# Kernel tuning notes

Measured on AMD Instinct MI355X. Metric: run time of the kernel, lower is better.

The kernel has to match this reference:

```python
import jax, jax.numpy as jnp
import numpy as np

NUM_HEADS = 8
HEAD_DIM = 64
SR = 2
LN_EPS = 1e-5


def _ln(x, g, b):
    # LayerNorm over last dim (torch nn.LayerNorm, eps=1e-5)
    m = jnp.mean(x, axis=-1, keepdims=True)
    v = jnp.var(x, axis=-1, keepdims=True)
    return (x - m) * jax.lax.rsqrt(v + LN_EPS) * g + b


def setup_inputs() -> dict:
    key = jax.random.key(0)
    ks = jax.random.split(key, 8)
    B, N, C = 8, 4096, 512
    Cc = 512                      # cross_dim
    inner = NUM_HEADS * HEAD_DIM  # 512
    w = lambda k, shp: jax.random.normal(k, shp, jnp.float32) * 0.02
    return {
        "x": jax.random.normal(ks[0], (B, N, C), jnp.float32),
        "y": jax.random.normal(ks[1], (B, 64 * 64, Cc), jnp.float32),
        "Wq": w(ks[2], (C, inner)),
        "Wkv": w(ks[3], (Cc, 2 * inner)),
        "Wproj": w(ks[4], (inner, C)),
        "bproj": jnp.zeros((C,), jnp.float32),
        "g_cross": jnp.ones((Cc,), jnp.float32),
        "b_cross": jnp.zeros((Cc,), jnp.float32),
        "sr_w": w(ks[5], (SR, SR, Cc, Cc)),   # HWIO conv kernel
        "sr_b": jnp.zeros((Cc,), jnp.float32),
        "g_sr": jnp.ones((Cc,), jnp.float32),
        "b_sr": jnp.zeros((Cc,), jnp.float32),
        "y_H": 64,
        "y_W": 64,
    }


def reference(x, y, Wq, Wkv, Wproj, bproj, g_cross, b_cross, sr_w, sr_b, g_sr, b_sr, y_H, y_W):
    B, N, C = x.shape
    h, d = NUM_HEADS, HEAD_DIM
    inner = h * d
    scale = d ** -0.5

    # q projection: [B, h, N, d]
    q = (x @ Wq).reshape(B, N, h, d).transpose(0, 2, 1, 3)

    # cross-attention norm on context
    y = _ln(y, g_cross, b_cross)
    Cc = y.shape[-1]

    # spatial reduction: conv(kernel=stride=SR) over [B, y_H, y_W, Cc]
    x_ = y.reshape(B, y_H, y_W, Cc)
    x_ = jax.lax.conv_general_dilated(
        x_, sr_w, window_strides=(SR, SR), padding='VALID',
        dimension_numbers=('NHWC', 'HWIO', 'NHWC')) + sr_b
    Nk = (y_H // SR) * (y_W // SR)
    x_ = _ln(x_.reshape(B, Nk, Cc), g_sr, b_sr)

    # kv projection: [2, B, h, Nk, d]
    kv = (x_ @ Wkv).reshape(B, Nk, 2, h, d).transpose(2, 0, 3, 1, 4)
    k, v = kv[0], kv[1]

    attn = jax.nn.softmax(jnp.einsum('bhnd,bhmd->bhnm', q, k) * scale, axis=-1)
    out = jnp.einsum('bhnm,bhmd->bhnd', attn, v)          # [B, h, N, d]
    out = out.transpose(0, 2, 1, 3).reshape(B, N, inner)  # [B, N, inner]
    return out @ Wproj + bproj
```

## Files before the change

kernel.cpp:

```cpp
#include <hip/hip_runtime.h>
#include <stdint.h>

typedef unsigned short u16;
typedef __attribute__((ext_vector_type(8))) short bf16x8;
typedef __attribute__((ext_vector_type(8))) unsigned short u16x8;
typedef __attribute__((ext_vector_type(4))) float f32x4;
typedef __attribute__((ext_vector_type(16))) float f32x16;
typedef __attribute__((ext_vector_type(4))) unsigned short u16x4;
typedef __attribute__((ext_vector_type(2))) unsigned int uint2v;

__device__ __forceinline__ u16 f2bf(float f) {
  unsigned u = __float_as_uint(f);
  u += 0x7fffu + ((u >> 16) & 1u);
  return (u16)(u >> 16);
}

__device__ __forceinline__ unsigned cvtpk(float lo, float hi) {
  unsigned r;
  asm("v_cvt_pk_bf16_f32 %0, %1, %2" : "=v"(r) : "v"(lo), "v"(hi));
  return r;
}

__device__ __forceinline__ void gload16(const u16* g, u16* l) {
  __builtin_amdgcn_global_load_lds(
      (const __attribute__((address_space(1))) unsigned int*)(uintptr_t)g,
      (__attribute__((address_space(3))) unsigned int*)(uintptr_t)l, 16, 0, 0);
}

__global__ __launch_bounds__(256) void transpose4_bf16(
    const float* __restrict__ W0, const float* __restrict__ W1,
    const float* __restrict__ W2, const float* __restrict__ W3,
    u16* __restrict__ T0, u16* __restrict__ T1, u16* __restrict__ T2,
    u16* __restrict__ T3) {
  __shared__ u16 lds[64][66];
  const float* W;
  u16* T;
  int R, C;
  switch (blockIdx.y) {
    case 0: W = W0; T = T0; R = 512; C = 512; break;
    case 1: W = W1; T = T1; R = 512; C = 1024; break;
    case 2: W = W2; T = T2; R = 512; C = 512; break;
    default: W = W3; T = T3; R = 2048; C = 512; break;
  }
  const int tilesC = C >> 6;
  const int nt = (R >> 6) * tilesC;
  const int tile = blockIdx.x;
  if (tile >= nt) return;
  const int tr = tile / tilesC, tc = tile - tr * tilesC;
  const int r0 = tr << 6, c0 = tc << 6;
  const int t = threadIdx.x;
  const int rr = t >> 2, cq = (t & 3) << 4;
  const float* src = W + (size_t)(r0 + rr) * C + c0 + cq;
  unsigned* ldsrow = (unsigned*)&lds[rr][cq];
#pragma unroll
  for (int j = 0; j < 4; j++) {
    f32x4 v = *(const f32x4*)(src + j * 4);
    ldsrow[j * 2] = cvtpk(v.x, v.y);
    ldsrow[j * 2 + 1] = cvtpk(v.z, v.w);
  }
  __syncthreads();
  const int oc = t >> 2, rq = (t & 3) << 4;
  u16x8 o0, o1;
#pragma unroll
  for (int j = 0; j < 8; j++) {
    o0[j] = lds[rq + j][oc];
    o1[j] = lds[rq + 8 + j][oc];
  }
  u16* dst = T + (size_t)(c0 + oc) * R + r0 + rq;
  *(u16x8*)dst = o0;
  *(u16x8*)(dst + 8) = o1;
}

__global__ __launch_bounds__(256) void cvt_bf16(const float* __restrict__ in,
                                                u16* __restrict__ out, int n4) {
  int i = blockIdx.x * 256 + threadIdx.x;
  if (i >= n4) return;
  f32x4 v = *(const f32x4*)(in + (size_t)i * 4);
  u16x4 o;
  o.x = f2bf(v.x); o.y = f2bf(v.y); o.z = f2bf(v.z); o.w = f2bf(v.w);
  *(u16x4*)(out + (size_t)i * 4) = o;
}

__global__ __launch_bounds__(256) void ln_y_im2col(
    const float* __restrict__ y, const float* __restrict__ g,
    const float* __restrict__ bb, u16* __restrict__ patches) {
  int row = blockIdx.x * 4 + (threadIdx.x >> 6);
  int l = threadIdx.x & 63;
  const float* yr = y + (size_t)row * 512;
  f32x4 v0 = *(const f32x4*)(yr + l * 4);
  f32x4 v1 = *(const f32x4*)(yr + 256 + l * 4);
  float s = v0.x + v0.y + v0.z + v0.w + v1.x + v1.y + v1.z + v1.w;
  float ss = v0.x * v0.x + v0.y * v0.y + v0.z * v0.z + v0.w * v0.w +
             v1.x * v1.x + v1.y * v1.y + v1.z * v1.z + v1.w * v1.w;
#pragma unroll
  for (int m = 1; m <= 32; m <<= 1) {
    s += __shfl_xor(s, m);
    ss += __shfl_xor(ss, m);
  }
  float mean = s * (1.0f / 512.0f);
  float inv = rsqrtf(ss * (1.0f / 512.0f) - mean * mean + 1e-5f);
  f32x4 g0 = *(const f32x4*)(g + l * 4), g1 = *(const f32x4*)(g + 256 + l * 4);
  f32x4 c0 = *(const f32x4*)(bb + l * 4), c1 = *(const f32x4*)(bb + 256 + l * 4);
  f32x4 o0 = (v0 - mean) * inv * g0 + c0;
  f32x4 o1 = (v1 - mean) * inv * g1 + c1;
  int b = row >> 12, n = row & 4095, r = n >> 6, cc = n & 63;
  u16* dst = patches +
             (size_t)((b << 10) + ((r >> 1) << 5) + (cc >> 1)) * 2048 +
             ((r & 1) * 2 + (cc & 1)) * 512;
  u16x4 w0, w1;
  w0.x = f2bf(o0.x); w0.y = f2bf(o0.y); w0.z = f2bf(o0.z); w0.w = f2bf(o0.w);
  w1.x = f2bf(o1.x); w1.y = f2bf(o1.y); w1.z = f2bf(o1.z); w1.w = f2bf(o1.w);
  *(u16x4*)(dst + l * 4) = w0;
  *(u16x4*)(dst + 256 + l * 4) = w1;
}

__global__ __launch_bounds__(256) void ln_rows(
    const float* __restrict__ in, const float* __restrict__ g,
    const float* __restrict__ bb, u16* __restrict__ out) {
  int row = blockIdx.x * 4 + (threadIdx.x >> 6);
  int l = threadIdx.x & 63;
  const float* xr = in + (size_t)row * 512;
  f32x4 v0 = *(const f32x4*)(xr + l * 4);
  f32x4 v1 = *(const f32x4*)(xr + 256 + l * 4);
  float s = v0.x + v0.y + v0.z + v0.w + v1.x + v1.y + v1.z + v1.w;
  float ss = v0.x * v0.x + v0.y * v0.y + v0.z * v0.z + v0.w * v0.w +
             v1.x * v1.x + v1.y * v1.y + v1.z * v1.z + v1.w * v1.w;
#pragma unroll
  for (int m = 1; m <= 32; m <<= 1) {
    s += __shfl_xor(s, m);
    ss += __shfl_xor(ss, m);
  }
  float mean = s * (1.0f / 512.0f);
  float inv = rsqrtf(ss * (1.0f / 512.0f) - mean * mean + 1e-5f);
  f32x4 g0 = *(const f32x4*)(g + l * 4), g1 = *(const f32x4*)(g + 256 + l * 4);
  f32x4 c0 = *(const f32x4*)(bb + l * 4), c1 = *(const f32x4*)(bb + 256 + l * 4);
  f32x4 o0 = (v0 - mean) * inv * g0 + c0;
  f32x4 o1 = (v1 - mean) * inv * g1 + c1;
  u16* dst = out + (size_t)row * 512;
  u16x4 w0, w1;
  w0.x = f2bf(o0.x); w0.y = f2bf(o0.y); w0.z = f2bf(o0.z); w0.w = f2bf(o0.w);
  w1.x = f2bf(o1.x); w1.y = f2bf(o1.y); w1.z = f2bf(o1.z); w1.w = f2bf(o1.w);
  *(u16x4*)(dst + l * 4) = w0;
  *(u16x4*)(dst + 256 + l * 4) = w1;
}

template <int EPI>
__global__ __launch_bounds__(256) void gemm_bt(
    const u16* __restrict__ A, const u16* __restrict__ BT, int M, int N, int K,
    float* __restrict__ OF, u16* __restrict__ OB, const float* __restrict__ bias,
    float scale, u16* __restrict__ KB, u16* __restrict__ VT) {
  __shared__ u16 As[2][128 * 32];
  __shared__ u16 Bs[2][128 * 32];
  const int tid = threadIdx.x;
  const int l = tid & 63, w = tid >> 6;
  const int brow = blockIdx.y * 128, bcol = blockIdx.x * 128;
  const int wr = w >> 1, wc = w & 1;
  const int lr = l & 15, lk = (l >> 4) * 8;
  const int srow = l >> 2, scol = (l & 3) * 8;
  const int r0s = w * 32 + srow, r1s = w * 32 + 16 + srow;
  const u16* Ap0 = &A[(size_t)(brow + r0s) * K + scol];
  const u16* Ap1 = &A[(size_t)(brow + r1s) * K + scol];
  const u16* Bp0 = &BT[(size_t)(bcol + r0s) * K + scol];
  const u16* Bp1 = &BT[(size_t)(bcol + r1s) * K + scol];
  const int lo0 = r0s * 32 + scol, lo1 = r1s * 32 + scol;
  f32x4 acc[4][4] = {};
  const int nt = K >> 5;
  gload16(Ap0, &As[0][lo0]);
  gload16(Ap1, &As[0][lo1]);
  gload16(Bp0, &Bs[0][lo0]);
  gload16(Bp1, &Bs[0][lo1]);
  __syncthreads();
  int cur = 0;
  for (int t = 0; t < nt; ++t) {
    if (t + 1 < nt) {
      int k0 = (t + 1) << 5;
      gload16(Ap0 + k0, &As[cur ^ 1][lo0]);
      gload16(Ap1 + k0, &As[cur ^ 1][lo1]);
      gload16(Bp0 + k0, &Bs[cur ^ 1][lo0]);
      gload16(Bp1 + k0, &Bs[cur ^ 1][lo1]);
    }
    bf16x8 af[4], bfr[4];
#pragma unroll
    for (int m = 0; m < 4; m++)
      af[m] = *(const bf16x8*)&As[cur][(wr * 64 + m * 16 + lr) * 32 + lk];
#pragma unroll
    for (int n = 0; n < 4; n++)
      bfr[n] = *(const bf16x8*)&Bs[cur][(wc * 64 + n * 16 + lr) * 32 + lk];
#pragma unroll
    for (int m = 0; m < 4; m++)
#pragma unroll
      for (int n = 0; n < 4; n++)
        acc[m][n] = __builtin_amdgcn_mfma_f32_16x16x32_bf16(af[m], bfr[n],
                                                            acc[m][n], 0, 0, 0);
    __syncthreads();
    cur ^= 1;
  }
#pragma unroll
  for (int m = 0; m < 4; m++) {
    int r0 = brow + wr * 64 + m * 16 + (l >> 4) * 4;
#pragma unroll
    for (int n = 0; n < 4; n++) {
      int c = bcol + wc * 64 + n * 16 + lr;
#pragma unroll
      for (int j = 0; j < 4; j++) {
        float v = acc[m][n][j];
        int rrow = r0 + j;
        if (EPI == 0) {
          OF[(size_t)rrow * N + c] = v + bias[c];
        } else if (EPI == 2) {
          OB[(size_t)rrow * N + c] = f2bf(v * scale);
        } else {
          int b = rrow >> 10, nn = rrow & 1023;
          int dd = c & 63;
          if (c < 512) {
            int hh = c >> 6;
            KB[((size_t)((b * 8 + hh) * 1024 + nn)) * 64 + dd] = f2bf(v);
          } else {
            int hh = (c - 512) >> 6;
            VT[((size_t)((b * 8 + hh) * 64 + dd)) * 1024 + nn] = f2bf(v);
          }
        }
      }
    }
  }
}

__global__ __launch_bounds__(256) void gemm_bt64(
    const u16* __restrict__ A, const u16* __restrict__ BT, int M, int N, int K,
    float* __restrict__ OF, const float* __restrict__ bias) {
  __shared__ u16 As[2][64 * 32];
  __shared__ u16 Bs[2][128 * 32];
  const int tid = threadIdx.x;
  const int l = tid & 63, w = tid >> 6;
  const int brow = blockIdx.y * 64, bcol = blockIdx.x * 128;
  const int lr = l & 15, lk = (l >> 4) * 8;
  const int srow = tid >> 2, scol = (tid & 3) * 8;
  const u16* Ap = &A[(size_t)(brow + srow) * K + scol];
  const u16* Bp0 = &BT[(size_t)(bcol + srow) * K + scol];
  const u16* Bp1 = &BT[(size_t)(bcol + 64 + srow) * K + scol];
  const int loA = srow * 32 + scol;
  const int loB1 = (64 + srow) * 32 + scol;
  f32x4 acc[4][2] = {};
  const int nt = K >> 5;
  gload16(Ap, &As[0][loA]);
  gload16(Bp0, &Bs[0][loA]);
  gload16(Bp1, &Bs[0][loB1]);
  __syncthreads();
  int cur = 0;
  for (int t = 0; t < nt; ++t) {
    if (t + 1 < nt) {
      int k0 = (t + 1) << 5;
      gload16(Ap + k0, &As[cur ^ 1][loA]);
      gload16(Bp0 + k0, &Bs[cur ^ 1][loA]);
      gload16(Bp1 + k0, &Bs[cur ^ 1][loB1]);
    }
    bf16x8 af[4], bfr[2];
#pragma unroll
    for (int m = 0; m < 4; m++)
      af[m] = *(const bf16x8*)&As[cur][(m * 16 + lr) * 32 + lk];
#pragma unroll
    for (int n = 0; n < 2; n++)
      bfr[n] = *(const bf16x8*)&Bs[cur][(w * 32 + n * 16 + lr) * 32 + lk];
#pragma unroll
    for (int m = 0; m < 4; m++)
#pragma unroll
      for (int n = 0; n < 2; n++)
        acc[m][n] = __builtin_amdgcn_mfma_f32_16x16x32_bf16(af[m], bfr[n],
                                                            acc[m][n], 0, 0, 0);
    __syncthreads();
    cur ^= 1;
  }
#pragma unroll
  for (int m = 0; m < 4; m++) {
    int r0 = brow + m * 16 + (l >> 4) * 4;
#pragma unroll
    for (int n = 0; n < 2; n++) {
      int c = bcol + w * 32 + n * 16 + lr;
#pragma unroll
      for (int j = 0; j < 4; j++)
        OF[(size_t)(r0 + j) * N + c] = acc[m][n][j] + bias[c];
    }
  }
}

__global__ __launch_bounds__(256) void attn_fwd(
    const u16* __restrict__ q, const u16* __restrict__ kb,
    const u16* __restrict__ vt, u16* __restrict__ o) {
  __shared__ u16 Ks[2][32 * 64];
  __shared__ u16 Vs[2][64 * 32];
  const int idx = blockIdx.x;
  const int bh = ((idx >> 7) << 3) | (idx & 7);
  const int qb = (idx >> 3) & 15;
  const int b = bh >> 3, h = bh & 7;
  const int tid = threadIdx.x;
  const int w = tid >> 6, l = tid & 63;
  const int lq = l & 31, hi = l >> 5;
  const int qrowA = qb * 256 + w * 64 + lq;
  const int qrowB = qrowA + 32;
  const u16* qpA = q + (size_t)((b << 12) + qrowA) * 512 + h * 64 + hi * 8;
  const u16* qpB = q + (size_t)((b << 12) + qrowB) * 512 + h * 64 + hi * 8;
  bf16x8 qfA[4], qfB[4];
#pragma unroll
  for (int ds = 0; ds < 4; ds++) {
    qfA[ds] = *(const bf16x8*)(qpA + ds * 16);
    qfB[ds] = *(const bf16x8*)(qpB + ds * 16);
  }
  const short one = 0x3F80;
  const bf16x8 ones = {one, one, one, one, one, one, one, one};
  const u16* kp = kb + (size_t)bh * 65536;
  const u16* vtb = vt + (size_t)bh * 65536;
  const int krow = tid >> 3, kslot = tid & 7;
  const u16* ksrc = kp + krow * 64 + ((kslot ^ (krow & 7)) << 3);
  const int vrow = tid >> 2, vslot = tid & 3;
  const u16* vsrc = vtb + (size_t)vrow * 1024 + ((vslot ^ ((vrow >> 1) & 3)) << 3);
  const int kOff0 = lq * 64;
  const int vOff0 = lq * 32;
  const int vOff1 = (lq + 32) * 32;
  const int vmask = (lq >> 1) & 3;
  f32x16 oA0 = {}, oA1 = {}, oB0 = {}, oB1 = {};
  f32x16 smA = {}, smB = {};
  gload16(ksrc, &Ks[0][tid << 3]);
  gload16(vsrc, &Vs[0][tid << 3]);
  __syncthreads();
  int cur = 0;
  for (int kv0 = 0; kv0 < 1024; kv0 += 32) {
    if (kv0 + 32 < 1024) {
      gload16(ksrc + (kv0 + 32) * 64, &Ks[cur ^ 1][tid << 3]);
      gload16(vsrc + (kv0 + 32), &Vs[cur ^ 1][tid << 3]);
    }
    bf16x8 kf[4];
#pragma unroll
    for (int ds = 0; ds < 4; ds++)
      kf[ds] = *(const bf16x8*)&Ks[cur][kOff0 + ((((ds << 1) + hi) ^ (lq & 7)) << 3)];
    bf16x8 vf0[2], vf1[2];
#pragma unroll
    for (int t = 0; t < 2; t++) {
      int sw = (((t << 1) + hi) ^ vmask) << 3;
      vf0[t] = *(const bf16x8*)&Vs[cur][vOff0 + sw];
      vf1[t] = *(const bf16x8*)&Vs[cur][vOff1 + sw];
    }
    f32x16 stA = {}, stB = {};
#pragma unroll
    for (int ds = 0; ds < 4; ds++) {
      stA = __builtin_amdgcn_mfma_f32_32x32x16_bf16(kf[ds], qfA[ds], stA, 0, 0, 0);
      stB = __builtin_amdgcn_mfma_f32_32x32x16_bf16(kf[ds], qfB[ds], stB, 0, 0, 0);
    }
    bf16x8 pbA[2], pbB[2];
#pragma unroll
    for (int tile = 0; tile < 2; tile++) {
      f32x16& st = tile ? stB : stA;
      bf16x8* pb = tile ? pbB : pbA;
      float p[16];
#pragma unroll
      for (int r = 0; r < 16; r++) p[r] = __builtin_amdgcn_exp2f(st[r]);
#pragma unroll
      for (int t = 0; t < 2; t++) {
        unsigned c0 = cvtpk(p[8 * t + 0], p[8 * t + 1]);
        unsigned c1 = cvtpk(p[8 * t + 2], p[8 * t + 3]);
        unsigned c2 = cvtpk(p[8 * t + 4], p[8 * t + 5]);
        unsigned c3 = cvtpk(p[8 * t + 6], p[8 * t + 7]);
        uint2v r02 = __builtin_amdgcn_permlane32_swap(c0, c2, false, false);
        uint2v r13 = __builtin_amdgcn_permlane32_swap(c1, c3, false, false);
        union {
          unsigned u[4];
          bf16x8 v;
        } pk;
        pk.u[0] = r02.x;
        pk.u[1] = r13.x;
        pk.u[2] = r02.y;
        pk.u[3] = r13.y;
        pb[t] = pk.v;
      }
    }
#pragma unroll
    for (int t = 0; t < 2; t++) {
      oA0 = __builtin_amdgcn_mfma_f32_32x32x16_bf16(vf0[t], pbA[t], oA0, 0, 0, 0);
      oA1 = __builtin_amdgcn_mfma_f32_32x32x16_bf16(vf1[t], pbA[t], oA1, 0, 0, 0);
      smA = __builtin_amdgcn_mfma_f32_32x32x16_bf16(ones, pbA[t], smA, 0, 0, 0);
      oB0 = __builtin_amdgcn_mfma_f32_32x32x16_bf16(vf0[t], pbB[t], oB0, 0, 0, 0);
      oB1 = __builtin_amdgcn_mfma_f32_32x32x16_bf16(vf1[t], pbB[t], oB1, 0, 0, 0);
      smB = __builtin_amdgcn_mfma_f32_32x32x16_bf16(ones, pbB[t], smB, 0, 0, 0);
    }
    __syncthreads();
    cur ^= 1;
  }
  const float invA = 1.0f / smA[0], invB = 1.0f / smB[0];
  u16* opA = o + (size_t)((b << 12) + qrowA) * 512 + h * 64;
  u16* opB = o + (size_t)((b << 12) + qrowB) * 512 + h * 64;
#pragma unroll
  for (int g = 0; g < 4; g++) {
    u16x4 a0, a1, b0, b1;
#pragma unroll
    for (int j = 0; j < 4; j++) {
      a0[j] = f2bf(oA0[g * 4 + j] * invA);
      a1[j] = f2bf(oA1[g * 4 + j] * invA);
      b0[j] = f2bf(oB0[g * 4 + j] * invB);
      b1[j] = f2bf(oB1[g * 4 + j] * invB);
    }
    *(u16x4*)(opA + 8 * g + 4 * hi) = a0;
    *(u16x4*)(opA + 32 + 8 * g + 4 * hi) = a1;
    *(u16x4*)(opB + 8 * g + 4 * hi) = b0;
    *(u16x4*)(opB + 32 + 8 * g + 4 * hi) = b1;
  }
}

extern "C" void kernel_launch(void* const* d_in, const int* in_sizes, int n_in,
                              void* d_out, int out_size, void* d_ws, size_t ws_size,
                              hipStream_t stream) {
  (void)in_sizes; (void)n_in; (void)out_size; (void)ws_size;
  const float* x = (const float*)d_in[0];
  const float* y = (const float*)d_in[1];
  const float* Wq = (const float*)d_in[2];
  const float* Wkv = (const float*)d_in[3];
  const float* Wproj = (const float*)d_in[4];
  const float* bproj = (const float*)d_in[5];
  const float* g_cross = (const float*)d_in[6];
  const float* b_cross = (const float*)d_in[7];
  const float* srw = (const float*)d_in[8];
  const float* sr_b = (const float*)d_in[9];
  const float* g_sr = (const float*)d_in[10];
  const float* b_sr = (const float*)d_in[11];
  float* out = (float*)d_out;

  u16* p = (u16*)d_ws;
  u16* WqT = p;    p += (size_t)512 * 512;
  u16* WkvT = p;   p += (size_t)1024 * 512;
  u16* WprojT = p; p += (size_t)512 * 512;
  u16* srwT = p;   p += (size_t)512 * 2048;
  u16* kbuf = p;   p += (size_t)8 * 8 * 1024 * 64;
  u16* vtbuf = p;  p += (size_t)8 * 8 * 1024 * 64;
  u16* xln = p;    p += (size_t)8192 * 512;
  u16* R1 = p;     p += (size_t)32768 * 512;
  u16* R2 = p;     p += (size_t)32768 * 512;
  u16* patches = R1;
  u16* xbf = R1;
  u16* attnb = R1;
  float* convout = (float*)R2;
  u16* qbuf = R2;

  transpose4_bf16<<<dim3(256, 4), 256, 0, stream>>>(Wq, Wkv, Wproj, srw,
                                                    WqT, WkvT, WprojT, srwT);
  ln_y_im2col<<<8192, 256, 0, stream>>>(y, g_cross, b_cross, patches);
  gemm_bt64<<<dim3(4, 128), 256, 0, stream>>>(patches, srwT, 8192, 512, 2048,
                                              convout, sr_b);
  ln_rows<<<2048, 256, 0, stream>>>(convout, g_sr, b_sr, xln);
  gemm_bt<1><<<dim3(8, 64), 256, 0, stream>>>(xln, WkvT, 8192, 1024, 512,
                                              nullptr, nullptr, nullptr, 1.0f,
                                              kbuf, vtbuf);
  cvt_bf16<<<16384, 256, 0, stream>>>(x, xbf, 32768 * 512 / 4);
  gemm_bt<2><<<dim3(4, 256), 256, 0, stream>>>(xbf, WqT, 32768, 512, 512,
                                               nullptr, qbuf, nullptr,
                                               0.125f * 1.44269504f,
                                               nullptr, nullptr);
  attn_fwd<<<dim3(1024), 256, 0, stream>>>(qbuf, kbuf, vtbuf, attnb);
  gemm_bt<0><<<dim3(4, 256), 256, 0, stream>>>(attnb, WprojT, 32768, 512, 512,
                                               out, nullptr, bproj, 1.0f,
                                               nullptr, nullptr);
}
```

Measured before the change: 277.6 us.

## Use triple-buffered LDS with vmcnt waits and one barrier per iteration

```diff
diff --git a/kernel.cpp b/kernel.cpp
--- a/kernel.cpp
+++ b/kernel.cpp
@@ -26,6 +26,11 @@
       (const __attribute__((address_space(1))) unsigned int*)(uintptr_t)g,
       (__attribute__((address_space(3))) unsigned int*)(uintptr_t)l, 16, 0, 0);
 }
+
+#define WAITV(N) asm volatile("s_waitcnt vmcnt(" #N ")" ::: "memory")
+#define BARRIER_FENCE()                  \
+  __builtin_amdgcn_s_barrier();          \
+  __builtin_amdgcn_sched_barrier(0)
 
 __global__ __launch_bounds__(256) void transpose4_bf16(
     const float* __restrict__ W0, const float* __restrict__ W1,
@@ -149,8 +154,8 @@
     const u16* __restrict__ A, const u16* __restrict__ BT, int M, int N, int K,
     float* __restrict__ OF, u16* __restrict__ OB, const float* __restrict__ bias,
     float scale, u16* __restrict__ KB, u16* __restrict__ VT) {
-  __shared__ u16 As[2][128 * 32];
-  __shared__ u16 Bs[2][128 * 32];
+  __shared__ u16 As[3][128 * 32];
+  __shared__ u16 Bs[3][128 * 32];
   const int tid = threadIdx.x;
   const int l = tid & 63, w = tid >> 6;
   const int brow = blockIdx.y * 128, bcol = blockIdx.x * 128;
@@ -169,31 +174,37 @@
   gload16(Ap1, &As[0][lo1]);
   gload16(Bp0, &Bs[0][lo0]);
   gload16(Bp1, &Bs[0][lo1]);
-  __syncthreads();
-  int cur = 0;
+  gload16(Ap0 + 32, &As[1][lo0]);
+  gload16(Ap1 + 32, &As[1][lo1]);
+  gload16(Bp0 + 32, &Bs[1][lo0]);
+  gload16(Bp1 + 32, &Bs[1][lo1]);
+  int bufC = 0, bufS = 2;
   for (int t = 0; t < nt; ++t) {
-    if (t + 1 < nt) {
-      int k0 = (t + 1) << 5;
-      gload16(Ap0 + k0, &As[cur ^ 1][lo0]);
-      gload16(Ap1 + k0, &As[cur ^ 1][lo1]);
-      gload16(Bp0 + k0, &Bs[cur ^ 1][lo0]);
-      gload16(Bp1 + k0, &Bs[cur ^ 1][lo1]);
+    if (t + 1 < nt) WAITV(4);
+    else WAITV(0);
+    BARRIER_FENCE();
+    if (t + 2 < nt) {
+      int k0 = (t + 2) << 5;
+      gload16(Ap0 + k0, &As[bufS][lo0]);
+      gload16(Ap1 + k0, &As[bufS][lo1]);
+      gload16(Bp0 + k0, &Bs[bufS][lo0]);
+      gload16(Bp1 + k0, &Bs[bufS][lo1]);
     }
     bf16x8 af[4], bfr[4];
 #pragma unroll
     for (int m = 0; m < 4; m++)
-      af[m] = *(const bf16x8*)&As[cur][(wr * 64 + m * 16 + lr) * 32 + lk];
+      af[m] = *(const bf16x8*)&As[bufC][(wr * 64 + m * 16 + lr) * 32 + lk];
 #pragma unroll
     for (int n = 0; n < 4; n++)
-      bfr[n] = *(const bf16x8*)&Bs[cur][(wc * 64 + n * 16 + lr) * 32 + lk];
+      bfr[n] = *(const bf16x8*)&Bs[bufC][(wc * 64 + n * 16 + lr) * 32 + lk];
 #pragma unroll
     for (int m = 0; m < 4; m++)
 #pragma unroll
       for (int n = 0; n < 4; n++)
         acc[m][n] = __builtin_amdgcn_mfma_f32_16x16x32_bf16(af[m], bfr[n],
                                                             acc[m][n], 0, 0, 0);
-    __syncthreads();
-    cur ^= 1;
+    bufC = bufC == 2 ? 0 : bufC + 1;
+    bufS = bufS == 2 ? 0 : bufS + 1;
   }
 #pragma unroll
   for (int m = 0; m < 4; m++) {
@@ -228,8 +239,8 @@
 __global__ __launch_bounds__(256) void gemm_bt64(
     const u16* __restrict__ A, const u16* __restrict__ BT, int M, int N, int K,
     float* __restrict__ OF, const float* __restrict__ bias) {
-  __shared__ u16 As[2][64 * 32];
-  __shared__ u16 Bs[2][128 * 32];
+  __shared__ u16 As[3][64 * 32];
+  __shared__ u16 Bs[3][128 * 32];
   const int tid = threadIdx.x;
   const int l = tid & 63, w = tid >> 6;
   const int brow = blockIdx.y * 64, bcol = blockIdx.x * 128;
@@ -245,30 +256,35 @@
   gload16(Ap, &As[0][loA]);
   gload16(Bp0, &Bs[0][loA]);
   gload16(Bp1, &Bs[0][loB1]);
-  __syncthreads();
-  int cur = 0;
+  gload16(Ap + 32, &As[1][loA]);
+  gload16(Bp0 + 32, &Bs[1][loA]);
+  gload16(Bp1 + 32, &Bs[1][loB1]);
+  int bufC = 0, bufS = 2;
   for (int t = 0; t < nt; ++t) {
-    if (t + 1 < nt) {
-      int k0 = (t + 1) << 5;
-      gload16(Ap + k0, &As[cur ^ 1][loA]);
-      gload16(Bp0 + k0, &Bs[cur ^ 1][loA]);
-      gload16(Bp1 + k0, &Bs[cur ^ 1][loB1]);
+    if (t + 1 < nt) WAITV(3);
+    else WAITV(0);
+    BARRIER_FENCE();
+    if (t + 2 < nt) {
+      int k0 = (t + 2) << 5;
+      gload16(Ap + k0, &As[bufS][loA]);
+      gload16(Bp0 + k0, &Bs[bufS][loA]);
+      gload16(Bp1 + k0, &Bs[bufS][loB1]);
     }
     bf16x8 af[4], bfr[2];
 #pragma unroll
     for (int m = 0; m < 4; m++)
-      af[m] = *(const bf16x8*)&As[cur][(m * 16 + lr) * 32 + lk];
+      af[m] = *(const bf16x8*)&As[bufC][(m * 16 + lr) * 32 + lk];
 #pragma unroll
     for (int n = 0; n < 2; n++)
-      bfr[n] = *(const bf16x8*)&Bs[cur][(w * 32 + n * 16 + lr) * 32 + lk];
+      bfr[n] = *(const bf16x8*)&Bs[bufC][(w * 32 + n * 16 + lr) * 32 + lk];
 #pragma unroll
     for (int m = 0; m < 4; m++)
 #pragma unroll
       for (int n = 0; n < 2; n++)
         acc[m][n] = __builtin_amdgcn_mfma_f32_16x16x32_bf16(af[m], bfr[n],
                                                             acc[m][n], 0, 0, 0);
-    __syncthreads();
-    cur ^= 1;
+    bufC = bufC == 2 ? 0 : bufC + 1;
+    bufS = bufS == 2 ? 0 : bufS + 1;
   }
 #pragma unroll
   for (int m = 0; m < 4; m++) {
@@ -286,8 +302,8 @@
 __global__ __launch_bounds__(256) void attn_fwd(
     const u16* __restrict__ q, const u16* __restrict__ kb,
     const u16* __restrict__ vt, u16* __restrict__ o) {
-  __shared__ u16 Ks[2][32 * 64];
-  __shared__ u16 Vs[2][64 * 32];
+  __shared__ u16 Ks[3][32 * 64];
+  __shared__ u16 Vs[3][64 * 32];
   const int idx = blockIdx.x;
   const int bh = ((idx >> 7) << 3) | (idx & 7);
   const int qb = (idx >> 3) & 15;
@@ -321,23 +337,30 @@
   f32x16 smA = {}, smB = {};
   gload16(ksrc, &Ks[0][tid << 3]);
   gload16(vsrc, &Vs[0][tid << 3]);
-  __syncthreads();
-  int cur = 0;
-  for (int kv0 = 0; kv0 < 1024; kv0 += 32) {
-    if (kv0 + 32 < 1024) {
-      gload16(ksrc + (kv0 + 32) * 64, &Ks[cur ^ 1][tid << 3]);
-      gload16(vsrc + (kv0 + 32), &Vs[cur ^ 1][tid << 3]);
-    }
+  gload16(ksrc + 32 * 64, &Ks[1][tid << 3]);
+  gload16(vsrc + 32, &Vs[1][tid << 3]);
+  int bufC = 0, bufS = 2;
+  for (int it = 0; it < 32; ++it) {
+    if (it < 31) WAITV(2);
+    else WAITV(0);
+    BARRIER_FENCE();
+    if (it + 2 < 32) {
+      int kv2 = (it + 2) << 5;
+      gload16(ksrc + kv2 * 64, &Ks[bufS][tid << 3]);
+      gload16(vsrc + kv2, &Vs[bufS][tid << 3]);
+    }
+    const u16* Kc = Ks[bufC];
+    const u16* Vc = Vs[bufC];
     bf16x8 kf[4];
 #pragma unroll
     for (int ds = 0; ds < 4; ds++)
-      kf[ds] = *(const bf16x8*)&Ks[cur][kOff0 + ((((ds << 1) + hi) ^ (lq & 7)) << 3)];
+      kf[ds] = *(const bf16x8*)&Kc[kOff0 + ((((ds << 1) + hi) ^ (lq & 7)) << 3)];
     bf16x8 vf0[2], vf1[2];
 #pragma unroll
     for (int t = 0; t < 2; t++) {
       int sw = (((t << 1) + hi) ^ vmask) << 3;
-      vf0[t] = *(const bf16x8*)&Vs[cur][vOff0 + sw];
-      vf1[t] = *(const bf16x8*)&Vs[cur][vOff1 + sw];
+      vf0[t] = *(const bf16x8*)&Vc[vOff0 + sw];
+      vf1[t] = *(const bf16x8*)&Vc[vOff1 + sw];
     }
     f32x16 stA = {}, stB = {};
 #pragma unroll
@@ -381,8 +404,8 @@
       oB1 = __builtin_amdgcn_mfma_f32_32x32x16_bf16(vf1[t], pbB[t], oB1, 0, 0, 0);
       smB = __builtin_amdgcn_mfma_f32_32x32x16_bf16(ones, pbB[t], smB, 0, 0, 0);
     }
-    __syncthreads();
-    cur ^= 1;
+    bufC = bufC == 2 ? 0 : bufC + 1;
+    bufS = bufS == 2 ? 0 : bufS + 1;
   }
   const float invA = 1.0f / smA[0], invB = 1.0f / smB[0];
   u16* opA = o + (size_t)((b << 12) + qrowA) * 512 + h * 64;
```

Result: faster. 250.3 us (-9.8%).
